# Kernel optimization log

Hardware: AMD Instinct MI355X
Metric: run time of the kernel (lower is better)

## Reference

```python
import jax, jax.numpy as jnp
import numpy as np

B, HH, WW, C = 16, 64, 64, 256
HEADS, DIM_K, DIM_U, DIM_OUT = 4, 16, 1, 256
DIM_V = DIM_OUT // HEADS  # 64
R = 23
EPS = 1e-3  # keras BatchNormalization default epsilon


def setup_inputs() -> dict:
    key = jax.random.key(0)
    ks = jax.random.split(key, 14)
    def n(i, shape, s=1.0):
        return jax.random.normal(ks[i], shape, dtype=jnp.float32) * s
    def u(i, shape):
        return jax.random.uniform(ks[i], shape, jnp.float32, 0.5, 1.5)
    return {
        "x": n(0, (B, HH, WW, C)),
        "Wq": n(1, (C, DIM_K * HEADS), 0.05),
        "Wk": n(2, (C, DIM_K * DIM_U), 0.05),
        "Wv": n(3, (C, DIM_V * DIM_U), 0.05),
        "gamma_q": u(4, (DIM_K * HEADS,)),
        "beta_q": n(5, (DIM_K * HEADS,), 0.1),
        "mean_q": n(6, (DIM_K * HEADS,), 0.1),
        "var_q": u(7, (DIM_K * HEADS,)),
        "gamma_v": u(8, (DIM_V * DIM_U,)),
        "beta_v": n(9, (DIM_V * DIM_U,), 0.1),
        "mean_v": n(10, (DIM_V * DIM_U,), 0.1),
        "var_v": u(11, (DIM_V * DIM_U,)),
        "pos_w": n(12, (1, R, R, DIM_U, DIM_K), 0.05),  # DHWIO, depth dim = v
        "pos_b": jnp.zeros((DIM_K,), jnp.float32),
    }


def reference(x, Wq, Wk, Wv, gamma_q, beta_q, mean_q, var_q,
              gamma_v, beta_v, mean_v, var_v, pos_w, pos_b):
    b = x.shape[0]
    n_pos = HH * WW
    # 1x1 conv projections = channel matmuls
    q = jnp.einsum('bhwc,cd->bhwd', x, Wq)
    k = jnp.einsum('bhwc,cd->bhwd', x, Wk)
    v = jnp.einsum('bhwc,cd->bhwd', x, Wv)
    # BatchNorm (inference mode: moving stats)
    q = (q - mean_q) * jax.lax.rsqrt(var_q + EPS) * gamma_q + beta_q
    v = (v - mean_v) * jax.lax.rsqrt(var_v + EPS) * gamma_v + beta_v
    # rearranges
    q = q.reshape(b, n_pos, HEADS, DIM_K).transpose(0, 2, 3, 1)    # b h k n
    k = k.reshape(b, n_pos, DIM_U, DIM_K).transpose(0, 2, 3, 1)    # b u k n
    v4 = v.reshape(b, n_pos, DIM_U, DIM_V).transpose(0, 2, 3, 1)   # b u v n
    k = jax.nn.softmax(k, axis=-1)  # softmax over positions
    # content lambda
    Lc = jnp.einsum('bukm,buvm->bkv', k, v4)
    Yc = jnp.einsum('bhkn,bkv->bnhv', q, Lc)
    # positional lambda via local Conv3D over (v, hh, ww) with u channels
    v5 = v4.reshape(b, DIM_U, DIM_V, HH, WW).transpose(0, 2, 3, 4, 1)  # b v hh ww u
    Lp = jax.lax.conv_general_dilated(
        v5, pos_w, window_strides=(1, 1, 1), padding='SAME',
        dimension_numbers=('NDHWC', 'DHWIO', 'NDHWC')) + pos_b         # b v hh ww k
    Lp = Lp.transpose(0, 1, 4, 2, 3).reshape(b, DIM_V, DIM_K, n_pos)   # b v k n
    Yp = jnp.einsum('bhkn,bvkn->bnhv', q, Lp)
    Y = Yc + Yp                                                        # b n h v
    return Y.reshape(b, HH, WW, HEADS * DIM_V)
```

## Files before the change

kernel.cpp:

```cpp
#include <hip/hip_runtime.h>
#include <stdint.h>

typedef __bf16 bf16x8 __attribute__((ext_vector_type(8)));
typedef float  f32x4  __attribute__((ext_vector_type(4)));
typedef float  f32x16 __attribute__((ext_vector_type(16)));
typedef unsigned short u16;

#define WCT_OFF   0u
#define SC_OFF    73728u
#define SH_OFF    74304u
#define BST_OFF   75008u
#define ZB_OFF    524288u
#define MSUM_OFF  640256u
#define LCB_OFF   642304u
#define QP_OFF    707840u
#define KT_OFF    9096448u
#define VT_OFF    11193600u
#define P_OFF     19582208u

__global__ void kP(const float* Wq, const float* Wk, const float* Wv,
                   const float* gq, const float* bq, const float* mq, const float* vq,
                   const float* gv, const float* bv, const float* mv, const float* vvar,
                   const float* pw, char* ws) {
  int t = threadIdx.x;
  int blk = blockIdx.x;
  if (blk < 144) {
    int n = blk, c = t;
    float val;
    if (n < 64)      val = Wq[c * 64 + n];
    else if (n < 80) val = Wk[c * 16 + (n - 64)];
    else             val = Wv[c * 64 + (n - 80)];
    ((__bf16*)(ws + WCT_OFF))[n * 256 + c] = (__bf16)val;
  } else if (blk == 144) {
    if (t < 144) {
      float s, sh;
      if (t < 64)      { s = gq[t] * rsqrtf(vq[t] + 1e-3f); sh = bq[t] - mq[t] * s; }
      else if (t < 80) { s = 1.f; sh = 0.f; }
      else { int i = t - 80; s = gv[i] * rsqrtf(vvar[i] + 1e-3f); sh = bv[i] - mv[i] * s; }
      ((float*)(ws + SC_OFF))[t] = s;
      ((float*)(ws + SH_OFF))[t] = sh;
    }
    f32x4 fz;
    fz[0] = 0.f; fz[1] = 0.f; fz[2] = 0.f; fz[3] = 0.f;
    *(f32x4*)(ws + ZB_OFF + t * 16) = fz;
  } else {
    int dy = blk - 145;
    __bf16* bst = (__bf16*)(ws + BST_OFF) + dy * 8192;
    for (int i = 0; i < 32; ++i) {
      int idx = i * 256 + t;
      int nt = idx >> 10;
      int w2 = (idx >> 9) & 1;
      int l  = (idx >> 3) & 63;
      int e  = idx & 7;
      int n  = nt * 32 + (l & 31);
      int xr = n >> 4, kch = n & 15;
      int o1 = (2 * nt + 5) & ~7;
      int j  = o1 + w2 * 16 + (l >> 5) * 8 + e;
      int dxw = j - xr - 5;
      float val = (dxw >= 0 && dxw < 23) ? pw[(dy * 23 + dxw) * 16 + kch] : 0.f;
      bst[idx] = (__bf16)val;
    }
  }
}

__global__ __launch_bounds__(256) void kA(const float* x, char* ws) {
  __shared__ __align__(16) u16 qlds[64 * 72];
  int t = threadIdx.x, w = t >> 6, l = t & 63;
  int m0 = blockIdx.x * 64;
  int b = m0 >> 12;
  int posb = m0 & 4095;
  const __bf16* wct = (const __bf16*)(ws + WCT_OFF);
  const float* sc = (const float*)(ws + SC_OFF);
  const float* sh = (const float*)(ws + SH_OFF);
  __bf16* qp = (__bf16*)(ws + QP_OFF);
  __bf16* kt = (__bf16*)(ws + KT_OFF);
  __bf16* vt = (__bf16*)(ws + VT_OFF);

  int rl = l & 15;
  int kg = l >> 4;

  f32x4 acc[9];
#pragma unroll
  for (int nf = 0; nf < 9; ++nf)
#pragma unroll
    for (int q = 0; q < 4; ++q) acc[nf][q] = 0.f;

  for (int ks = 0; ks < 8; ++ks) {
    int m = m0 + w * 16 + rl;
    const float* xp = x + (size_t)m * 256 + ks * 32 + kg * 8;
    f32x4 v0 = *(const f32x4*)xp;
    f32x4 v1 = *(const f32x4*)(xp + 4);
    bf16x8 a;
    a[0] = (__bf16)v0[0]; a[1] = (__bf16)v0[1]; a[2] = (__bf16)v0[2]; a[3] = (__bf16)v0[3];
    a[4] = (__bf16)v1[0]; a[5] = (__bf16)v1[1]; a[6] = (__bf16)v1[2]; a[7] = (__bf16)v1[3];
#pragma unroll
    for (int nf = 0; nf < 9; ++nf) {
      bf16x8 bfr = *(const bf16x8*)(wct + (nf * 16 + rl) * 256 + ks * 32 + kg * 8);
      acc[nf] = __builtin_amdgcn_mfma_f32_16x16x32_bf16(a, bfr, acc[nf], 0, 0, 0);
    }
  }

#pragma unroll
  for (int nf = 0; nf < 9; ++nf) {
    int ch = nf * 16 + rl;
    float s = sc[ch], shv = sh[ch];
    int pbase = w * 16 + kg * 4;
    union { __bf16 h[4]; uint2 u; } pk;
#pragma unroll
    for (int r = 0; r < 4; ++r) pk.h[r] = (__bf16)(acc[nf][r] * s + shv);
    if (ch < 64) {
#pragma unroll
      for (int r = 0; r < 4; ++r)
        qlds[(pbase + r) * 72 + ch] = ((u16*)&pk.h[r])[0];
    } else if (ch < 80) {
      *(uint2*)(kt + (size_t)(b * 16 + ch - 64) * 4096 + posb + pbase) = pk.u;
    } else {
      *(uint2*)(vt + (size_t)(b * 64 + ch - 80) * 4096 + posb + pbase) = pk.u;
    }
  }
  __syncthreads();
#pragma unroll
  for (int i = 0; i < 2; ++i) {
    int chunk = t + i * 256;
    int row = chunk >> 3, seg = chunk & 7;
    bf16x8 vq_ = *(const bf16x8*)(qlds + row * 72 + seg * 8);
    *(bf16x8*)(qp + (size_t)(b * 4096 + posb + row) * 64 + seg * 8) = vq_;
  }
}

__global__ void kB1(char* ws) {
  __shared__ float red[256];
  int t = threadIdx.x;
  int b = blockIdx.x >> 4, kk = blockIdx.x & 15;
  const __bf16* kt = (const __bf16*)(ws + KT_OFF) + (size_t)(b * 16 + kk) * 4096;
  __bf16* P = (__bf16*)(ws + P_OFF) + (size_t)(b * 16 + kk) * 4096;
  float v[16];
  bf16x8 c0 = *(const bf16x8*)(kt + t * 16);
  bf16x8 c1 = *(const bf16x8*)(kt + t * 16 + 8);
#pragma unroll
  for (int i = 0; i < 8; ++i) { v[i] = (float)c0[i]; v[8 + i] = (float)c1[i]; }
  float mx = v[0];
#pragma unroll
  for (int i = 1; i < 16; ++i) mx = fmaxf(mx, v[i]);
  red[t] = mx; __syncthreads();
  for (int s = 128; s > 0; s >>= 1) { if (t < s) red[t] = fmaxf(red[t], red[t + s]); __syncthreads(); }
  mx = red[0]; __syncthreads();
  float se = 0.f;
  union { __bf16 h[8]; uint4 u; } p0, p1;
#pragma unroll
  for (int i = 0; i < 8; ++i) { float e = expf(v[i] - mx); se += e; p0.h[i] = (__bf16)e; }
#pragma unroll
  for (int i = 0; i < 8; ++i) { float e = expf(v[8 + i] - mx); se += e; p1.h[i] = (__bf16)e; }
  *(uint4*)(P + t * 16) = p0.u;
  *(uint4*)(P + t * 16 + 8) = p1.u;
  red[t] = se; __syncthreads();
  for (int s = 128; s > 0; s >>= 1) { if (t < s) red[t] += red[t + s]; __syncthreads(); }
  if (t == 0) {
    float* ms = (float*)(ws + MSUM_OFF);
    ms[(b * 16 + kk) * 2] = mx;
    ms[(b * 16 + kk) * 2 + 1] = 1.f / red[0];
  }
}

__global__ __launch_bounds__(256) void kB2(char* ws, const float* pos_b) {
  __shared__ float red[16][256];
  int t = threadIdx.x;
  int b = blockIdx.x >> 6, v = blockIdx.x & 63;
  const __bf16* P = (const __bf16*)(ws + P_OFF) + (size_t)b * 16 * 4096;
  const __bf16* vt = (const __bf16*)(ws + VT_OFF) + (size_t)(b * 64 + v) * 4096;
  const float* ms = (const float*)(ws + MSUM_OFF) + b * 32;
  float acc[16];
#pragma unroll
  for (int i = 0; i < 16; ++i) acc[i] = 0.f;
  for (int c = 0; c < 16; ++c) {
    int p = c * 256 + t;
    float vv = (float)vt[p];
#pragma unroll
    for (int i = 0; i < 16; ++i)
      acc[i] += (float)P[i * 4096 + p] * vv;
  }
#pragma unroll
  for (int i = 0; i < 16; ++i) red[i][t] = acc[i];
  __syncthreads();
  for (int s = 128; s > 0; s >>= 1) {
    if (t < s) {
#pragma unroll
      for (int i = 0; i < 16; ++i) red[i][t] += red[i][t + s];
    }
    __syncthreads();
  }
  if (t < 16) {
    float* lcb = (float*)(ws + LCB_OFF);
    lcb[(b * 16 + t) * 64 + v] = red[t][0] * ms[2 * t + 1] + pos_b[t];
  }
}

__global__ __launch_bounds__(512, 4) void kC(char* ws, float* out) {
  __shared__ __align__(16) u16 img[3][64][64];
  __shared__ __align__(16) u16 bbuf[3][8192];
  __shared__ __align__(16) u16 qt[2048];
  int t = threadIdx.x, w = t >> 6, l = t & 63;
  int bid = blockIdx.x;
  int swz = (bid & 7) * 256 + (bid >> 3);
  int b = swz >> 7;
  int rest = swz & 127;
  int yp = rest >> 2, xt = rest & 3;
  int y0 = yp * 2, x0g = xt * 16;
  const __bf16* vt  = (const __bf16*)(ws + VT_OFF);
  const __bf16* qp  = (const __bf16*)(ws + QP_OFF);
  const float*  lcb = (const float*)(ws + LCB_OFF) + b * 1024;
  const char*   bstc = (const char*)(ws + BST_OFF);
  const char*   zb   = (const char*)(ws + ZB_OFF) + (t & 255) * 16;

  int yy = w >> 2, ntp = w & 3;
  int hh = l >> 5;
  int o1_8 = ((4 * ntp + 5) & ~7) >> 3;

  int sv = t >> 3, sc8 = t & 7;
  int sgx = x0g - 16 + (sc8 ^ (sv & 7)) * 8;
  bool sokx = (sgx >= 0 && sgx < 64);
  const char* vsrc = (const char*)(vt + (size_t)(b * 64 + sv) * 4096 + sgx);

#define STAGE_IMG(slot, rowv) do {                                             \
    int _r = (rowv);                                                           \
    const char* _s = (sokx && _r >= 0 && _r < 64) ? (vsrc + _r * 128) : zb;    \
    __builtin_amdgcn_global_load_lds(                                          \
      (const __attribute__((address_space(1))) void*)_s,                       \
      (__attribute__((address_space(3))) void*)((char*)&img[0][0][0] + (slot) * 8192 + w * 1024), \
      16, 0, 0);                                                               \
  } while (0)

#define STAGE_B(bufsel, dyv) do {                                              \
    const char* gsrc = bstc + (dyv) * 16384 + w * 1024 + l * 16;               \
    char* ldsb = (char*)&bbuf[0][0] + (bufsel) * 16384 + w * 1024;             \
    _Pragma("unroll")                                                          \
    for (int i_ = 0; i_ < 2; ++i_)                                             \
      __builtin_amdgcn_global_load_lds(                                        \
        (const __attribute__((address_space(1))) void*)(gsrc + i_ * 8192),     \
        (__attribute__((address_space(3))) void*)(ldsb + i_ * 8192), 16, 0, 0);\
  } while (0)

  STAGE_IMG(0, y0 - 11);
  STAGE_IMG(1, y0 - 10);
  STAGE_B(0, 0);
  STAGE_B(1, 1);
  {
    int f0 = t * 4;
    int qyy = f0 >> 10, qx = (f0 >> 6) & 15, qch = f0 & 63;
    *(uint2*)&qt[f0] =
      *(const uint2*)(qp + (size_t)(b * 4096 + (y0 + qyy) * 64 + x0g + qx) * 64 + qch);
  }
  asm volatile("s_waitcnt lgkmcnt(0)" ::: "memory");

  int boff[2][2];
#pragma unroll
  for (int j = 0; j < 2; ++j)
#pragma unroll
    for (int w2 = 0; w2 < 2; ++w2)
      boff[j][w2] = ((((2 * ntp + j) * 2 + w2) * 64) + l) * 8;

  f32x16 acc[2][2];
#pragma unroll
  for (int mf = 0; mf < 2; ++mf)
#pragma unroll
    for (int j = 0; j < 2; ++j)
#pragma unroll
      for (int q = 0; q < 16; ++q) acc[mf][j][q] = 0.f;

  int cur = 0;
  for (int dy = 0; dy < 23; ++dy) {
    int nxt = cur + 1; if (nxt == 3) nxt = 0;
    int wsl = nxt + 1; if (wsl == 3) wsl = 0;
    if (dy < 22) {
      asm volatile("s_waitcnt vmcnt(2)" ::: "memory");
    } else {
      asm volatile("s_waitcnt vmcnt(0)" ::: "memory");
    }
    __builtin_amdgcn_s_barrier();
    __builtin_amdgcn_sched_barrier(0);
    asm volatile("" ::: "memory");

    if (dy < 22) STAGE_IMG(wsl, y0 + dy - 9);
    if (dy < 21) STAGE_B(wsl, dy + 2);

    const u16* bq = &bbuf[0][0] + cur * 8192;
    int rsl = yy ? nxt : cur;
    bf16x8 af[2][2], bi[2][2];
#pragma unroll
    for (int j = 0; j < 2; ++j)
#pragma unroll
      for (int w2 = 0; w2 < 2; ++w2)
        af[j][w2] = *(const bf16x8*)(bq + boff[j][w2]);
#pragma unroll
    for (int mf = 0; mf < 2; ++mf) {
      int v = mf * 32 + (l & 31);
#pragma unroll
      for (int w2 = 0; w2 < 2; ++w2)
        bi[mf][w2] = *(const bf16x8*)(&img[rsl][v][((o1_8 + w2 * 2 + hh) ^ (v & 7)) * 8]);
    }
#pragma unroll
    for (int w2 = 0; w2 < 2; ++w2)
#pragma unroll
      for (int j = 0; j < 2; ++j) {
        acc[0][j] = __builtin_amdgcn_mfma_f32_32x32x16_bf16(af[j][w2], bi[0][w2], acc[0][j], 0, 0, 0);
        acc[1][j] = __builtin_amdgcn_mfma_f32_32x32x16_bf16(af[j][w2], bi[1][w2], acc[1][j], 0, 0, 0);
      }
    cur = nxt;
  }
#undef STAGE_IMG
#undef STAGE_B

  float lc[2][16];
#pragma unroll
  for (int mf = 0; mf < 2; ++mf)
#pragma unroll
    for (int r = 0; r < 16; ++r) {
      int k = (r & 3) + 8 * ((r >> 2) & 1) + 4 * hh;
      lc[mf][r] = lcb[k * 64 + mf * 32 + (l & 31)];
    }
  size_t obase = ((size_t)b * 4096 + (y0 + yy) * 64 + x0g) * 256;
#pragma unroll
  for (int j = 0; j < 2; ++j) {
#pragma unroll
    for (int xh = 0; xh < 2; ++xh) {
      int x_local = 2 * (2 * ntp + j) + xh;
      const u16* qrow = &qt[(yy * 16 + x_local) * 64];
#pragma unroll
      for (int h = 0; h < 4; ++h) {
        float s0 = 0.f, s1 = 0.f;
#pragma unroll
        for (int r8 = 0; r8 < 8; ++r8) {
          int r = xh * 8 + r8;
          int k = (r8 & 3) + 8 * (r8 >> 2) + 4 * hh;
          float qv = (float)(*(const __bf16*)&qrow[h * 16 + k]);
          s0 += qv * (acc[0][j][r] + lc[0][r]);
          s1 += qv * (acc[1][j][r] + lc[1][r]);
        }
        s0 += __shfl_xor(s0, 32);
        s1 += __shfl_xor(s1, 32);
        float val = (l >= 32) ? s1 : s0;
        out[obase + (size_t)x_local * 256 + h * 64 + l] = val;
      }
    }
  }
}

extern "C" void kernel_launch(void* const* d_in, const int* in_sizes, int n_in,
                              void* d_out, int out_size, void* d_ws, size_t ws_size,
                              hipStream_t stream) {
  const float* x   = (const float*)d_in[0];
  const float* Wq  = (const float*)d_in[1];
  const float* Wk  = (const float*)d_in[2];
  const float* Wv  = (const float*)d_in[3];
  const float* gq  = (const float*)d_in[4];
  const float* bq  = (const float*)d_in[5];
  const float* mq  = (const float*)d_in[6];
  const float* vq  = (const float*)d_in[7];
  const float* gv  = (const float*)d_in[8];
  const float* bv  = (const float*)d_in[9];
  const float* mv  = (const float*)d_in[10];
  const float* vvr = (const float*)d_in[11];
  const float* pw  = (const float*)d_in[12];
  const float* pb  = (const float*)d_in[13];
  char* ws = (char*)d_ws;
  float* out = (float*)d_out;

  hipLaunchKernelGGL(kP, dim3(168), dim3(256), 0, stream,
                     Wq, Wk, Wv, gq, bq, mq, vq, gv, bv, mv, vvr, pw, ws);
  hipLaunchKernelGGL(kA, dim3(1024), dim3(256), 0, stream, x, ws);
  hipLaunchKernelGGL(kB1, dim3(256), dim3(256), 0, stream, ws);
  hipLaunchKernelGGL(kB2, dim3(1024), dim3(256), 0, stream, ws, pb);
  hipLaunchKernelGGL(kC, dim3(2048), dim3(512), 0, stream, ws, out);
}
```

Baseline: 179.0 us.

## Read positional weight fragments from global memory instead of staging them in LDS

Drops the triple-buffered LDS staging of the per-dy positional-weight tiles. Each wave now loads its bf16x8 MFMA A-fragments straight from the global workspace, relying on L2/cache reuse across blocks. The image-row ring grows to four slots, prefetched one row further ahead, and the vmcnt wait is adjusted to match. This cuts LDS per block from roughly 100KB to 36KB, which can allow more resident blocks per CU, at the cost of global-load latency inside the inner dy loop.

```diff
diff --git a/kernel.cpp b/kernel.cpp
--- a/kernel.cpp
+++ b/kernel.cpp
@@ -196,8 +196,7 @@
 }
 
 __global__ __launch_bounds__(512, 4) void kC(char* ws, float* out) {
-  __shared__ __align__(16) u16 img[3][64][64];
-  __shared__ __align__(16) u16 bbuf[3][8192];
+  __shared__ __align__(16) u16 img[4][64][64];
   __shared__ __align__(16) u16 qt[2048];
   int t = threadIdx.x, w = t >> 6, l = t & 63;
   int bid = blockIdx.x;
@@ -230,20 +229,9 @@
       16, 0, 0);                                                               \
   } while (0)
 
-#define STAGE_B(bufsel, dyv) do {                                              \
-    const char* gsrc = bstc + (dyv) * 16384 + w * 1024 + l * 16;               \
-    char* ldsb = (char*)&bbuf[0][0] + (bufsel) * 16384 + w * 1024;             \
-    _Pragma("unroll")                                                          \
-    for (int i_ = 0; i_ < 2; ++i_)                                             \
-      __builtin_amdgcn_global_load_lds(                                        \
-        (const __attribute__((address_space(1))) void*)(gsrc + i_ * 8192),     \
-        (__attribute__((address_space(3))) void*)(ldsb + i_ * 8192), 16, 0, 0);\
-  } while (0)
-
   STAGE_IMG(0, y0 - 11);
   STAGE_IMG(1, y0 - 10);
-  STAGE_B(0, 0);
-  STAGE_B(1, 1);
+  STAGE_IMG(2, y0 - 9);
   {
     int f0 = t * 4;
     int qyy = f0 >> 10, qx = (f0 >> 6) & 15, qch = f0 & 63;
@@ -252,12 +240,12 @@
   }
   asm volatile("s_waitcnt lgkmcnt(0)" ::: "memory");
 
-  int boff[2][2];
+  int afoff[2][2];
 #pragma unroll
   for (int j = 0; j < 2; ++j)
 #pragma unroll
     for (int w2 = 0; w2 < 2; ++w2)
-      boff[j][w2] = ((((2 * ntp + j) * 2 + w2) * 64) + l) * 8;
+      afoff[j][w2] = ((((2 * ntp + j) * 2 + w2) * 64) + l) * 16;
 
   f32x16 acc[2][2];
 #pragma unroll
@@ -267,12 +255,9 @@
 #pragma unroll
       for (int q = 0; q < 16; ++q) acc[mf][j][q] = 0.f;
 
-  int cur = 0;
   for (int dy = 0; dy < 23; ++dy) {
-    int nxt = cur + 1; if (nxt == 3) nxt = 0;
-    int wsl = nxt + 1; if (wsl == 3) wsl = 0;
     if (dy < 22) {
-      asm volatile("s_waitcnt vmcnt(2)" ::: "memory");
+      asm volatile("s_waitcnt vmcnt(1)" ::: "memory");
     } else {
       asm volatile("s_waitcnt vmcnt(0)" ::: "memory");
     }
@@ -280,17 +265,17 @@
     __builtin_amdgcn_sched_barrier(0);
     asm volatile("" ::: "memory");
 
-    if (dy < 22) STAGE_IMG(wsl, y0 + dy - 9);
-    if (dy < 21) STAGE_B(wsl, dy + 2);
-
-    const u16* bq = &bbuf[0][0] + cur * 8192;
-    int rsl = yy ? nxt : cur;
+    if (dy < 21) STAGE_IMG((dy + 3) & 3, y0 + dy - 8);
+
+    const char* bdy = bstc + dy * 16384;
     bf16x8 af[2][2], bi[2][2];
 #pragma unroll
     for (int j = 0; j < 2; ++j)
 #pragma unroll
       for (int w2 = 0; w2 < 2; ++w2)
-        af[j][w2] = *(const bf16x8*)(bq + boff[j][w2]);
+        af[j][w2] = *(const bf16x8*)(bdy + afoff[j][w2]);
+
+    int rsl = (dy + yy) & 3;
 #pragma unroll
     for (int mf = 0; mf < 2; ++mf) {
       int v = mf * 32 + (l & 31);
@@ -305,10 +290,8 @@
         acc[0][j] = __builtin_amdgcn_mfma_f32_32x32x16_bf16(af[j][w2], bi[0][w2], acc[0][j], 0, 0, 0);
         acc[1][j] = __builtin_amdgcn_mfma_f32_32x32x16_bf16(af[j][w2], bi[1][w2], acc[1][j], 0, 0, 0);
       }
-    cur = nxt;
   }
 #undef STAGE_IMG
-#undef STAGE_B
 
   float lc[2][16];
 #pragma unroll
```

New measurement: 173.1 us. 3.3% less time.
